# Performance work log

Hardware: AMD Instinct MI355X
Metric: run time of the kernel (lower is better)

Reference implementation:

```python
import jax, jax.numpy as jnp
import numpy as np

D = 64          # d_in
NH = [256, 256] # nn_depth_design
L = 16          # flow_layers
B = 32768       # batch of samples


def _build_masks():
    # Deterministic mask maps: this_min=0, this_max=d_in-1 for all layers
    mh0 = np.arange(NH[0]) % (D - 1)
    mh1 = np.arange(NH[1]) % (D - 1)
    M1 = (mh0[None, :] <= mh1[:, None]).astype(np.float32)  # [nh1, nh0]
    M0s, M2s = [], []
    for l in range(L):
        perm = np.arange(D) if l % 2 == 0 else np.arange(D)[::-1]
        M0s.append((perm[None, :] <= mh0[:, None]).astype(np.float32))  # [nh0, D]
        M2s.append((mh1[None, :] < perm[:, None]).astype(np.float32))  # [D, nh1]
    M0 = np.stack(M0s)                                   # [L, nh0, D]
    M1 = np.broadcast_to(M1, (L,) + M1.shape).copy()     # [L, nh1, nh0]
    M2 = np.stack(M2s)                                   # [L, D, nh1]
    return jnp.asarray(M0), jnp.asarray(M1), jnp.asarray(M2)


def setup_inputs() -> dict:
    key = jax.random.key(0)
    ks = jax.random.split(key, 13)
    u = jax.random.normal(ks[0], (B, D), dtype=jnp.float32)

    def w(k, shape, fan_in):
        return jax.random.uniform(k, shape, jnp.float32, -1.0, 1.0) / np.sqrt(fan_in)

    inp = {"u": u}
    i = 1
    for net in ("loc", "scale"):
        inp[f"{net}_W0"] = w(ks[i], (L, NH[0], D), D); i += 1
        inp[f"{net}_b0"] = w(ks[i], (L, NH[0]), D); i += 1
        inp[f"{net}_W1"] = w(ks[i], (L, NH[1], NH[0]), NH[0]); i += 1
        inp[f"{net}_b1"] = w(ks[i], (L, NH[1]), NH[0]); i += 1
        inp[f"{net}_W2"] = w(ks[i], (L, D, NH[1]), NH[1]); i += 1
        inp[f"{net}_b2"] = w(ks[i], (L, D), NH[1]); i += 1
    M0, M1, M2 = _build_masks()
    inp["M0"], inp["M1"], inp["M2"] = M0, M1, M2
    return inp


def reference(u, loc_W0, loc_b0, loc_W1, loc_b1, loc_W2, loc_b2,
              scale_W0, scale_b0, scale_W1, scale_b1, scale_W2, scale_b2,
              M0, M1, M2):
    def step(y, p):
        (lW0, lb0, lW1, lb1, lW2, lb2,
         sW0, sb0, sW1, sb1, sW2, sb2, m0, m1, m2) = p

        def net(W0, b0, W1, b1, W2, b2):
            h = jax.nn.relu(y @ (m0 * W0).T + b0)    # [B, nh0]
            h = jax.nn.relu(h @ (m1 * W1).T + b1)    # [B, nh1]
            return h @ (m2 * W2).T + b2              # [B, D]

        loc = net(lW0, lb0, lW1, lb1, lW2, lb2)
        sc = net(sW0, sb0, sW1, sb1, sW2, sb2)
        # inverse=False coupling: exp(-scale) * (y - loc)
        return jnp.exp(-sc) * (y - loc), None

    params = (loc_W0, loc_b0, loc_W1, loc_b1, loc_W2, loc_b2,
              scale_W0, scale_b0, scale_W1, scale_b1, scale_W2, scale_b2,
              M0, M1, M2)
    y, _ = jax.lax.scan(step, u, params)
    return y
```

## Files before the change

### kernel.cpp

```cpp
#include <hip/hip_runtime.h>
#include <hip/hip_bf16.h>

typedef __bf16 bf16x8 __attribute__((ext_vector_type(8)));
typedef __bf16 bf16x4 __attribute__((ext_vector_type(4)));
typedef float  f32x4  __attribute__((ext_vector_type(4)));

#define LAYERS 16
#define DIM 64
#define NHID 256
#define BATCH 32768
#define MTILE 64
#define NBLOCKS (BATCH / MTILE)

#define W0P_PER 16384
#define W1P_PER 65536
#define W2P_PER 16384
#define W0P_TOT (32 * W0P_PER)
#define W1P_TOT (32 * W1P_PER)
#define W2P_TOT (32 * W2P_PER)
#define PACK_TOT (W0P_TOT + W1P_TOT + W2P_TOT)

__device__ __forceinline__ bf16x8 ldw(const __bf16* p) { return *(const bf16x8*)p; }

__device__ __forceinline__ void lds_barrier() {
    asm volatile("s_waitcnt lgkmcnt(0)" ::: "memory");
    __builtin_amdgcn_s_barrier();
    asm volatile("" ::: "memory");
}

__global__ __launch_bounds__(256) void pack_weights(
    const float* __restrict__ lW0, const float* __restrict__ lW1, const float* __restrict__ lW2,
    const float* __restrict__ sW0, const float* __restrict__ sW1, const float* __restrict__ sW2,
    __bf16* __restrict__ ws)
{
    const long i = ((long)blockIdx.x * 256 + threadIdx.x) * 8;
    const float* W; long src; int l, n, k, which;
    if (i < W0P_TOT) {
        int netl = (int)(i / W0P_PER), rem = (int)(i % W0P_PER);
        int net = netl >> 4; l = netl & 15;
        int nt = rem >> 10, kt = (rem >> 9) & 1, lane = (rem >> 3) & 63;
        n = nt * 16 + (lane & 15); k = kt * 32 + (lane >> 4) * 8;
        W = net ? sW0 : lW0; which = 0;
        src = (long)(l * 256 + n) * 64 + k;
    } else if (i < W0P_TOT + W1P_TOT) {
        long r = i - W0P_TOT;
        int netl = (int)(r / W1P_PER), rem = (int)(r % W1P_PER);
        int net = netl >> 4; l = netl & 15;
        int nt = rem >> 12, kt = (rem >> 9) & 7, lane = (rem >> 3) & 63;
        n = nt * 16 + (lane & 15); k = kt * 32 + (lane >> 4) * 8;
        W = net ? sW1 : lW1; which = 1;
        src = (long)(l * 256 + n) * 256 + k;
    } else {
        long r = i - W0P_TOT - W1P_TOT;
        int netl = (int)(r / W2P_PER), rem = (int)(r % W2P_PER);
        int net = netl >> 4; l = netl & 15;
        int nt = rem >> 12, kt = (rem >> 9) & 7, lane = (rem >> 3) & 63;
        n = nt * 16 + (lane & 15); k = kt * 32 + (lane >> 4) * 8;
        W = net ? sW2 : lW2; which = 2;
        src = (long)(l * 64 + n) * 256 + k;
    }
    f32x4 wa = *(const f32x4*)(W + src);
    f32x4 wb = *(const f32x4*)(W + src + 4);
    const int nm = n % 63;
    const int pn = (l & 1) ? 63 - n : n;
    bf16x8 o;
    #pragma unroll
    for (int j = 0; j < 8; ++j) {
        int kk = k + j;
        bool m;
        if (which == 0)      { int pk = (l & 1) ? 63 - kk : kk; m = (pk <= nm); }
        else if (which == 1) { m = ((kk % 63) <= nm); }
        else                 { m = ((kk % 63) < pn); }
        float v = (j < 4) ? wa[j] : wb[j - 4];
        o[j] = m ? (__bf16)v : (__bf16)0.0f;
    }
    *(bf16x8*)(ws + i) = o;
}

__global__ void __attribute__((amdgpu_flat_work_group_size(512, 512)))
                __attribute__((amdgpu_waves_per_eu(4)))
flow_kernel(
    const float* __restrict__ u,
    const __bf16* __restrict__ wp,
    const float* __restrict__ lb0, const float* __restrict__ lb1, const float* __restrict__ lb2,
    const float* __restrict__ sb0, const float* __restrict__ sb1, const float* __restrict__ sb2,
    float* __restrict__ out)
{
    __shared__ __bf16 ybf[4 * 2 * 512];
    __shared__ __bf16 buf1[4 * 8 * 512];
    __shared__ __bf16 buf2[4 * 8 * 512];

    const int tid  = threadIdx.x;
    const int w    = tid >> 6;
    const int lane = tid & 63;
    const int quad = lane >> 4;
    const int l16  = lane & 15;
    const int blk  = blockIdx.x;

    const int qh = quad >> 1;
    const int qp = (quad & 1) * 4;

    const int otD = w >> 1;
    const int bh  = w & 1;

    const __bf16* w0p = wp;
    const __bf16* w1p = wp + W0P_TOT;
    const __bf16* w2p = wp + W0P_TOT + W1P_TOT;

    f32x4 y[2];
    #pragma unroll
    for (int bt = 0; bt < 2; ++bt)
        y[bt] = *(const f32x4*)(u + (long)(blk * MTILE + bh * 32 + bt * 16 + l16) * DIM
                                  + otD * 16 + quad * 4);

    const int ktY = w >> 2;
    const int flY = ((((w >> 1) & 1) * 2 + qh) * 16 + l16);

    bf16x8 wg1[4];
    #pragma unroll
    for (int oi = 0; oi < 2; ++oi)
        #pragma unroll
        for (int kt = 0; kt < 2; ++kt)
            wg1[oi * 2 + kt] = ldw(w0p + (long)((2 * w + oi) * 2 + kt) * 512 + lane * 8);

    for (int l = 0; l < LAYERS; ++l) {
        #pragma unroll
        for (int bt = 0; bt < 2; ++bt) {
            bf16x4 v;
            #pragma unroll
            for (int r = 0; r < 4; ++r) v[r] = (__bf16)y[bt][r];
            *(bf16x4*)&ybf[(((bh * 2 + bt) * 2 + ktY) * 64 + flY) * 8 + qp] = v;
        }
        lds_barrier();

        #pragma unroll
        for (int net = 0; net < 2; ++net) {
            const __bf16* w1b = w1p + (long)(net * 16 + l) * W1P_PER;
            const __bf16* w2b = w2p + (long)(net * 16 + l) * W2P_PER;
            const __bf16* w0n = w0p + (long)(net == 0 ? 16 + l : l + 1) * W0P_PER;
            const float* b0 = (net ? sb0 : lb0) + l * 256;
            const float* b1 = (net ? sb1 : lb1) + l * 256;
            const float* b2 = (net ? sb2 : lb2) + l * 64;

            bf16x8 wg2a[8];

            {
                f32x4 acc[2][4];
                #pragma unroll
                for (int oi = 0; oi < 2; ++oi)
                    #pragma unroll
                    for (int bt = 0; bt < 4; ++bt)
                        acc[oi][bt] = (f32x4){0.f, 0.f, 0.f, 0.f};
                #pragma unroll
                for (int kt = 0; kt < 2; ++kt) {
                    bf16x8 bv[4];
                    #pragma unroll
                    for (int bt = 0; bt < 4; ++bt)
                        bv[bt] = *(const bf16x8*)&ybf[((bt * 2 + kt) * 64 + lane) * 8];
                    #pragma unroll
                    for (int oi = 0; oi < 2; ++oi)
                        #pragma unroll
                        for (int bt = 0; bt < 4; ++bt)
                            acc[oi][bt] = __builtin_amdgcn_mfma_f32_16x16x32_bf16(wg1[oi * 2 + kt], bv[bt], acc[oi][bt], 0, 0, 0);
                }
                #pragma unroll
                for (int kt = 0; kt < 4; ++kt)
                    #pragma unroll
                    for (int oi = 0; oi < 2; ++oi)
                        wg2a[kt * 2 + oi] = ldw(w1b + (long)((2 * w + oi) * 8 + kt) * 512 + lane * 8);
                #pragma unroll
                for (int oi = 0; oi < 2; ++oi) {
                    f32x4 bias = *(const f32x4*)(b0 + (2 * w + oi) * 16 + quad * 4);
                    const int fl = ((oi * 2 + qh) * 16 + l16);
                    #pragma unroll
                    for (int bt = 0; bt < 4; ++bt) {
                        bf16x4 v;
                        #pragma unroll
                        for (int r = 0; r < 4; ++r)
                            v[r] = (__bf16)fmaxf(acc[oi][bt][r] + bias[r], 0.f);
                        *(bf16x4*)&buf1[((bt * 8 + w) * 64 + fl) * 8 + qp] = v;
                    }
                }
            }
            lds_barrier();

            bf16x8 wg3[8];

            {
                f32x4 acc[2][4];
                #pragma unroll
                for (int oi = 0; oi < 2; ++oi)
                    #pragma unroll
                    for (int bt = 0; bt < 4; ++bt)
                        acc[oi][bt] = (f32x4){0.f, 0.f, 0.f, 0.f};
                #pragma unroll
                for (int kt = 0; kt < 8; ++kt) {
                    bf16x8 aw[2];
                    #pragma unroll
                    for (int oi = 0; oi < 2; ++oi)
                        aw[oi] = (kt < 4) ? wg2a[kt * 2 + oi]
                                          : ldw(w1b + (long)((2 * w + oi) * 8 + kt) * 512 + lane * 8);
                    bf16x8 bv[4];
                    #pragma unroll
                    for (int bt = 0; bt < 4; ++bt)
                        bv[bt] = *(const bf16x8*)&buf1[((bt * 8 + kt) * 64 + lane) * 8];
                    #pragma unroll
                    for (int oi = 0; oi < 2; ++oi)
                        #pragma unroll
                        for (int bt = 0; bt < 4; ++bt)
                            acc[oi][bt] = __builtin_amdgcn_mfma_f32_16x16x32_bf16(aw[oi], bv[bt], acc[oi][bt], 0, 0, 0);
                }
                #pragma unroll
                for (int oi = 0; oi < 2; ++oi) {
                    f32x4 bias = *(const f32x4*)(b1 + (2 * w + oi) * 16 + quad * 4);
                    const int fl = ((oi * 2 + qh) * 16 + l16);
                    #pragma unroll
                    for (int bt = 0; bt < 4; ++bt) {
                        bf16x4 v;
                        #pragma unroll
                        for (int r = 0; r < 4; ++r)
                            v[r] = (__bf16)fmaxf(acc[oi][bt][r] + bias[r], 0.f);
                        *(bf16x4*)&buf2[((bt * 8 + w) * 64 + fl) * 8 + qp] = v;
                    }
                }
                #pragma unroll
                for (int kt = 0; kt < 8; ++kt)
                    wg3[kt] = ldw(w2b + (long)(otD * 8 + kt) * 512 + lane * 8);
            }
            lds_barrier();

            {
                f32x4 acc3[2];
                #pragma unroll
                for (int bt = 0; bt < 2; ++bt)
                    acc3[bt] = (f32x4){0.f, 0.f, 0.f, 0.f};
                #pragma unroll
                for (int kt = 0; kt < 8; ++kt) {
                    #pragma unroll
                    for (int bt = 0; bt < 2; ++bt) {
                        bf16x8 bv = *(const bf16x8*)&buf2[(((bh * 2 + bt) * 8 + kt) * 64 + lane) * 8];
                        acc3[bt] = __builtin_amdgcn_mfma_f32_16x16x32_bf16(wg3[kt], bv, acc3[bt], 0, 0, 0);
                    }
                }
                #pragma unroll
                for (int oi = 0; oi < 2; ++oi)
                    #pragma unroll
                    for (int kt = 0; kt < 2; ++kt)
                        wg1[oi * 2 + kt] = ldw(w0n + (long)((2 * w + oi) * 2 + kt) * 512 + lane * 8);
                f32x4 bias = *(const f32x4*)(b2 + otD * 16 + quad * 4);
                if (net == 0) {
                    #pragma unroll
                    for (int bt = 0; bt < 2; ++bt)
                        #pragma unroll
                        for (int r = 0; r < 4; ++r)
                            y[bt][r] -= (acc3[bt][r] + bias[r]);
                } else {
                    #pragma unroll
                    for (int bt = 0; bt < 2; ++bt)
                        #pragma unroll
                        for (int r = 0; r < 4; ++r)
                            y[bt][r] = __expf(-(acc3[bt][r] + bias[r])) * y[bt][r];
                }
            }
        }
    }

    #pragma unroll
    for (int bt = 0; bt < 2; ++bt)
        *(f32x4*)(out + (long)(blk * MTILE + bh * 32 + bt * 16 + l16) * DIM
                      + otD * 16 + quad * 4) = y[bt];
}

extern "C" void kernel_launch(void* const* d_in, const int* in_sizes, int n_in,
                              void* d_out, int out_size, void* d_ws, size_t ws_size,
                              hipStream_t stream) {
    const float* u   = (const float*)d_in[0];
    const float* lW0 = (const float*)d_in[1];
    const float* lb0 = (const float*)d_in[2];
    const float* lW1 = (const float*)d_in[3];
    const float* lb1 = (const float*)d_in[4];
    const float* lW2 = (const float*)d_in[5];
    const float* lb2 = (const float*)d_in[6];
    const float* sW0 = (const float*)d_in[7];
    const float* sb0 = (const float*)d_in[8];
    const float* sW1 = (const float*)d_in[9];
    const float* sb1 = (const float*)d_in[10];
    const float* sW2 = (const float*)d_in[11];
    const float* sb2 = (const float*)d_in[12];

    if (ws_size < (size_t)PACK_TOT * sizeof(__bf16)) return;
    __bf16* ws = (__bf16*)d_ws;

    pack_weights<<<PACK_TOT / 8 / 256, 256, 0, stream>>>(
        lW0, lW1, lW2, sW0, sW1, sW2, ws);
    flow_kernel<<<NBLOCKS, 512, 0, stream>>>(
        u, ws, lb0, lb1, lb2, sb0, sb1, sb2, (float*)d_out);
}
```

Before: 299.4 us.

## Process loc and scale nets together per layer with half-size batch tiles

The batch tile drops from 64 to 32 rows and the loc and scale MLPs now run concurrently within one pass per layer, with waves split across the two nets instead of looping over them. Weights are repacked so each layer's loc and scale matrices sit together, and the second and third layer weight loads are software-pipelined through a rotating register buffer. This halves the number of barriers per layer and doubles the block count, at the cost of more weight traffic per sample because each block now covers fewer rows.

```diff
diff --git a/kernel.cpp b/kernel.cpp
--- a/kernel.cpp
+++ b/kernel.cpp
@@ -9,15 +9,15 @@
 #define DIM 64
 #define NHID 256
 #define BATCH 32768
-#define MTILE 64
+#define MTILE 32
 #define NBLOCKS (BATCH / MTILE)
 
-#define W0P_PER 16384
-#define W1P_PER 65536
-#define W2P_PER 16384
-#define W0P_TOT (32 * W0P_PER)
-#define W1P_TOT (32 * W1P_PER)
-#define W2P_TOT (32 * W2P_PER)
+#define W0P_PER 32768
+#define W1P_PER 131072
+#define W2P_PER 32768
+#define W0P_TOT (16 * W0P_PER)
+#define W1P_TOT (16 * W1P_PER)
+#define W2P_TOT (16 * W2P_PER)
 #define PACK_TOT (W0P_TOT + W1P_TOT + W2P_TOT)
 
 __device__ __forceinline__ bf16x8 ldw(const __bf16* p) { return *(const bf16x8*)p; }
@@ -36,26 +36,26 @@
     const long i = ((long)blockIdx.x * 256 + threadIdx.x) * 8;
     const float* W; long src; int l, n, k, which;
     if (i < W0P_TOT) {
-        int netl = (int)(i / W0P_PER), rem = (int)(i % W0P_PER);
-        int net = netl >> 4; l = netl & 15;
-        int nt = rem >> 10, kt = (rem >> 9) & 1, lane = (rem >> 3) & 63;
-        n = nt * 16 + (lane & 15); k = kt * 32 + (lane >> 4) * 8;
+        l = (int)(i / W0P_PER); int rem = (int)(i % W0P_PER);
+        int g = rem >> 3, lane = g & 63, kt = (g >> 6) & 1, ot = g >> 7;
+        int net = ot >> 4;
+        n = (ot & 15) * 16 + (lane & 15); k = kt * 32 + (lane >> 4) * 8;
         W = net ? sW0 : lW0; which = 0;
         src = (long)(l * 256 + n) * 64 + k;
     } else if (i < W0P_TOT + W1P_TOT) {
         long r = i - W0P_TOT;
-        int netl = (int)(r / W1P_PER), rem = (int)(r % W1P_PER);
-        int net = netl >> 4; l = netl & 15;
-        int nt = rem >> 12, kt = (rem >> 9) & 7, lane = (rem >> 3) & 63;
-        n = nt * 16 + (lane & 15); k = kt * 32 + (lane >> 4) * 8;
+        l = (int)(r / W1P_PER); int rem = (int)(r % W1P_PER);
+        int g = rem >> 3, lane = g & 63, kt = (g >> 6) & 7, ot = g >> 9;
+        int net = ot >> 4;
+        n = (ot & 15) * 16 + (lane & 15); k = kt * 32 + (lane >> 4) * 8;
         W = net ? sW1 : lW1; which = 1;
         src = (long)(l * 256 + n) * 256 + k;
     } else {
         long r = i - W0P_TOT - W1P_TOT;
-        int netl = (int)(r / W2P_PER), rem = (int)(r % W2P_PER);
-        int net = netl >> 4; l = netl & 15;
-        int nt = rem >> 12, kt = (rem >> 9) & 7, lane = (rem >> 3) & 63;
-        n = nt * 16 + (lane & 15); k = kt * 32 + (lane >> 4) * 8;
+        l = (int)(r / W2P_PER); int rem = (int)(r % W2P_PER);
+        int g = rem >> 3, lane = g & 63, kt = (g >> 6) & 7, ot = g >> 9;
+        int net = ot >> 2;
+        n = (ot & 3) * 16 + (lane & 15); k = kt * 32 + (lane >> 4) * 8;
         W = net ? sW2 : lW2; which = 2;
         src = (long)(l * 64 + n) * 256 + k;
     }
@@ -86,9 +86,9 @@
     const float* __restrict__ sb0, const float* __restrict__ sb1, const float* __restrict__ sb2,
     float* __restrict__ out)
 {
-    __shared__ __bf16 ybf[4 * 2 * 512];
-    __shared__ __bf16 buf1[4 * 8 * 512];
-    __shared__ __bf16 buf2[4 * 8 * 512];
+    __shared__ __bf16 ybf[2 * 2 * 512];
+    __shared__ __bf16 buf1[2 * 16 * 512];
+    __shared__ __bf16 buf2[2 * 16 * 512];
 
     const int tid  = threadIdx.x;
     const int w    = tid >> 6;
@@ -100,175 +100,159 @@
     const int qh = quad >> 1;
     const int qp = (quad & 1) * 4;
 
-    const int otD = w >> 1;
-    const int bh  = w & 1;
+    const int d    = w >> 1;
+    const int h    = w & 1;
+    const int net2 = w >> 2;
+    const int wm   = w & 3;
 
     const __bf16* w0p = wp;
     const __bf16* w1p = wp + W0P_TOT;
     const __bf16* w2p = wp + W0P_TOT + W1P_TOT;
 
-    f32x4 y[2];
+    f32x4 y = *(const f32x4*)(u + (long)(blk * MTILE + h * 16 + l16) * DIM
+                                + d * 16 + quad * 4);
+
+    const int ktY = d >> 1;
+    const int flY = ((d & 1) * 2 + qh) * 16 + l16;
+
+    bf16x8 wg1[8];
     #pragma unroll
-    for (int bt = 0; bt < 2; ++bt)
-        y[bt] = *(const f32x4*)(u + (long)(blk * MTILE + bh * 32 + bt * 16 + l16) * DIM
-                                  + otD * 16 + quad * 4);
-
-    const int ktY = w >> 2;
-    const int flY = ((((w >> 1) & 1) * 2 + qh) * 16 + l16);
-
-    bf16x8 wg1[4];
-    #pragma unroll
-    for (int oi = 0; oi < 2; ++oi)
+    for (int oi = 0; oi < 4; ++oi)
         #pragma unroll
         for (int kt = 0; kt < 2; ++kt)
-            wg1[oi * 2 + kt] = ldw(w0p + (long)((2 * w + oi) * 2 + kt) * 512 + lane * 8);
+            wg1[oi * 2 + kt] = ldw(w0p + (long)((4 * w + oi) * 2 + kt) * 512 + lane * 8);
 
     for (int l = 0; l < LAYERS; ++l) {
-        #pragma unroll
-        for (int bt = 0; bt < 2; ++bt) {
+        {
             bf16x4 v;
             #pragma unroll
-            for (int r = 0; r < 4; ++r) v[r] = (__bf16)y[bt][r];
-            *(bf16x4*)&ybf[(((bh * 2 + bt) * 2 + ktY) * 64 + flY) * 8 + qp] = v;
+            for (int r = 0; r < 4; ++r) v[r] = (__bf16)y[r];
+            *(bf16x4*)&ybf[((h * 2 + ktY) * 64 + flY) * 8 + qp] = v;
         }
         lds_barrier();
 
-        #pragma unroll
-        for (int net = 0; net < 2; ++net) {
-            const __bf16* w1b = w1p + (long)(net * 16 + l) * W1P_PER;
-            const __bf16* w2b = w2p + (long)(net * 16 + l) * W2P_PER;
-            const __bf16* w0n = w0p + (long)(net == 0 ? 16 + l : l + 1) * W0P_PER;
-            const float* b0 = (net ? sb0 : lb0) + l * 256;
-            const float* b1 = (net ? sb1 : lb1) + l * 256;
-            const float* b2 = (net ? sb2 : lb2) + l * 64;
-
-            bf16x8 wg2a[8];
-
-            {
-                f32x4 acc[2][4];
-                #pragma unroll
-                for (int oi = 0; oi < 2; ++oi)
-                    #pragma unroll
-                    for (int bt = 0; bt < 4; ++bt)
-                        acc[oi][bt] = (f32x4){0.f, 0.f, 0.f, 0.f};
-                #pragma unroll
-                for (int kt = 0; kt < 2; ++kt) {
-                    bf16x8 bv[4];
-                    #pragma unroll
-                    for (int bt = 0; bt < 4; ++bt)
-                        bv[bt] = *(const bf16x8*)&ybf[((bt * 2 + kt) * 64 + lane) * 8];
-                    #pragma unroll
-                    for (int oi = 0; oi < 2; ++oi)
-                        #pragma unroll
-                        for (int bt = 0; bt < 4; ++bt)
-                            acc[oi][bt] = __builtin_amdgcn_mfma_f32_16x16x32_bf16(wg1[oi * 2 + kt], bv[bt], acc[oi][bt], 0, 0, 0);
-                }
-                #pragma unroll
-                for (int kt = 0; kt < 4; ++kt)
-                    #pragma unroll
-                    for (int oi = 0; oi < 2; ++oi)
-                        wg2a[kt * 2 + oi] = ldw(w1b + (long)((2 * w + oi) * 8 + kt) * 512 + lane * 8);
-                #pragma unroll
-                for (int oi = 0; oi < 2; ++oi) {
-                    f32x4 bias = *(const f32x4*)(b0 + (2 * w + oi) * 16 + quad * 4);
-                    const int fl = ((oi * 2 + qh) * 16 + l16);
-                    #pragma unroll
-                    for (int bt = 0; bt < 4; ++bt) {
-                        bf16x4 v;
-                        #pragma unroll
-                        for (int r = 0; r < 4; ++r)
-                            v[r] = (__bf16)fmaxf(acc[oi][bt][r] + bias[r], 0.f);
-                        *(bf16x4*)&buf1[((bt * 8 + w) * 64 + fl) * 8 + qp] = v;
-                    }
-                }
-            }
-            lds_barrier();
-
-            bf16x8 wg3[8];
-
-            {
-                f32x4 acc[2][4];
-                #pragma unroll
-                for (int oi = 0; oi < 2; ++oi)
-                    #pragma unroll
-                    for (int bt = 0; bt < 4; ++bt)
-                        acc[oi][bt] = (f32x4){0.f, 0.f, 0.f, 0.f};
-                #pragma unroll
-                for (int kt = 0; kt < 8; ++kt) {
-                    bf16x8 aw[2];
-                    #pragma unroll
-                    for (int oi = 0; oi < 2; ++oi)
-                        aw[oi] = (kt < 4) ? wg2a[kt * 2 + oi]
-                                          : ldw(w1b + (long)((2 * w + oi) * 8 + kt) * 512 + lane * 8);
-                    bf16x8 bv[4];
-                    #pragma unroll
-                    for (int bt = 0; bt < 4; ++bt)
-                        bv[bt] = *(const bf16x8*)&buf1[((bt * 8 + kt) * 64 + lane) * 8];
-                    #pragma unroll
-                    for (int oi = 0; oi < 2; ++oi)
-                        #pragma unroll
-                        for (int bt = 0; bt < 4; ++bt)
-                            acc[oi][bt] = __builtin_amdgcn_mfma_f32_16x16x32_bf16(aw[oi], bv[bt], acc[oi][bt], 0, 0, 0);
-                }
-                #pragma unroll
-                for (int oi = 0; oi < 2; ++oi) {
-                    f32x4 bias = *(const f32x4*)(b1 + (2 * w + oi) * 16 + quad * 4);
-                    const int fl = ((oi * 2 + qh) * 16 + l16);
-                    #pragma unroll
-                    for (int bt = 0; bt < 4; ++bt) {
-                        bf16x4 v;
-                        #pragma unroll
-                        for (int r = 0; r < 4; ++r)
-                            v[r] = (__bf16)fmaxf(acc[oi][bt][r] + bias[r], 0.f);
-                        *(bf16x4*)&buf2[((bt * 8 + w) * 64 + fl) * 8 + qp] = v;
-                    }
-                }
-                #pragma unroll
-                for (int kt = 0; kt < 8; ++kt)
-                    wg3[kt] = ldw(w2b + (long)(otD * 8 + kt) * 512 + lane * 8);
-            }
-            lds_barrier();
-
-            {
-                f32x4 acc3[2];
+        const __bf16* w1b = w1p + (long)l * W1P_PER;
+        const __bf16* w2b = w2p + (long)l * W2P_PER;
+        const __bf16* w0n = w0p + (long)(l + 1) * W0P_PER;
+        const float* b0 = (net2 ? sb0 : lb0) + l * 256;
+        const float* b1 = (net2 ? sb1 : lb1) + l * 256;
+
+        bf16x8 wg2a[12];
+
+        {
+            f32x4 acc[4][2];
+            #pragma unroll
+            for (int oi = 0; oi < 4; ++oi)
                 #pragma unroll
                 for (int bt = 0; bt < 2; ++bt)
-                    acc3[bt] = (f32x4){0.f, 0.f, 0.f, 0.f};
-                #pragma unroll
-                for (int kt = 0; kt < 8; ++kt) {
-                    #pragma unroll
-                    for (int bt = 0; bt < 2; ++bt) {
-                        bf16x8 bv = *(const bf16x8*)&buf2[(((bh * 2 + bt) * 8 + kt) * 64 + lane) * 8];
-                        acc3[bt] = __builtin_amdgcn_mfma_f32_16x16x32_bf16(wg3[kt], bv, acc3[bt], 0, 0, 0);
-                    }
-                }
-                #pragma unroll
-                for (int oi = 0; oi < 2; ++oi)
-                    #pragma unroll
-                    for (int kt = 0; kt < 2; ++kt)
-                        wg1[oi * 2 + kt] = ldw(w0n + (long)((2 * w + oi) * 2 + kt) * 512 + lane * 8);
-                f32x4 bias = *(const f32x4*)(b2 + otD * 16 + quad * 4);
-                if (net == 0) {
-                    #pragma unroll
-                    for (int bt = 0; bt < 2; ++bt)
-                        #pragma unroll
-                        for (int r = 0; r < 4; ++r)
-                            y[bt][r] -= (acc3[bt][r] + bias[r]);
-                } else {
-                    #pragma unroll
-                    for (int bt = 0; bt < 2; ++bt)
-                        #pragma unroll
-                        for (int r = 0; r < 4; ++r)
-                            y[bt][r] = __expf(-(acc3[bt][r] + bias[r])) * y[bt][r];
-                }
-            }
+                    acc[oi][bt] = (f32x4){0.f, 0.f, 0.f, 0.f};
+            #pragma unroll
+            for (int kt = 0; kt < 2; ++kt)
+                #pragma unroll
+                for (int bt = 0; bt < 2; ++bt) {
+                    bf16x8 bv = *(const bf16x8*)&ybf[((bt * 2 + kt) * 64 + lane) * 8];
+                    #pragma unroll
+                    for (int oi = 0; oi < 4; ++oi)
+                        acc[oi][bt] = __builtin_amdgcn_mfma_f32_16x16x32_bf16(wg1[oi * 2 + kt], bv, acc[oi][bt], 0, 0, 0);
+                }
+            #pragma unroll
+            for (int s = 0; s < 3; ++s)
+                #pragma unroll
+                for (int oi = 0; oi < 4; ++oi)
+                    wg2a[s * 4 + oi] = ldw(w1b + (long)((4 * w + oi) * 8 + s) * 512 + lane * 8);
+            #pragma unroll
+            for (int oi = 0; oi < 4; ++oi) {
+                const int kt1 = 2 * wm + (oi >> 1) + 8 * net2;
+                const int fl  = ((oi & 1) * 2 + qh) * 16 + l16;
+                f32x4 bias = *(const f32x4*)(b0 + (4 * wm + oi) * 16 + quad * 4);
+                #pragma unroll
+                for (int bt = 0; bt < 2; ++bt) {
+                    bf16x4 v;
+                    #pragma unroll
+                    for (int r = 0; r < 4; ++r)
+                        v[r] = (__bf16)fmaxf(acc[oi][bt][r] + bias[r], 0.f);
+                    *(bf16x4*)&buf1[((bt * 16 + kt1) * 64 + fl) * 8 + qp] = v;
+                }
+            }
+        }
+        lds_barrier();
+
+        bf16x8 wg3[8];
+
+        {
+            f32x4 acc[4][2];
+            #pragma unroll
+            for (int oi = 0; oi < 4; ++oi)
+                #pragma unroll
+                for (int bt = 0; bt < 2; ++bt)
+                    acc[oi][bt] = (f32x4){0.f, 0.f, 0.f, 0.f};
+            #pragma unroll
+            for (int kt = 0; kt < 8; ++kt) {
+                const int slot = kt % 3;
+                #pragma unroll
+                for (int bt = 0; bt < 2; ++bt) {
+                    bf16x8 bv = *(const bf16x8*)&buf1[((bt * 16 + net2 * 8 + kt) * 64 + lane) * 8];
+                    #pragma unroll
+                    for (int oi = 0; oi < 4; ++oi)
+                        acc[oi][bt] = __builtin_amdgcn_mfma_f32_16x16x32_bf16(wg2a[slot * 4 + oi], bv, acc[oi][bt], 0, 0, 0);
+                }
+                if (kt < 5) {
+                    #pragma unroll
+                    for (int oi = 0; oi < 4; ++oi)
+                        wg2a[slot * 4 + oi] = ldw(w1b + (long)((4 * w + oi) * 8 + (kt + 3)) * 512 + lane * 8);
+                }
+            }
+            #pragma unroll
+            for (int oi = 0; oi < 4; ++oi) {
+                const int kt1 = 2 * wm + (oi >> 1) + 8 * net2;
+                const int fl  = ((oi & 1) * 2 + qh) * 16 + l16;
+                f32x4 bias = *(const f32x4*)(b1 + (4 * wm + oi) * 16 + quad * 4);
+                #pragma unroll
+                for (int bt = 0; bt < 2; ++bt) {
+                    bf16x4 v;
+                    #pragma unroll
+                    for (int r = 0; r < 4; ++r)
+                        v[r] = (__bf16)fmaxf(acc[oi][bt][r] + bias[r], 0.f);
+                    *(bf16x4*)&buf2[((bt * 16 + kt1) * 64 + fl) * 8 + qp] = v;
+                }
+            }
+            #pragma unroll
+            for (int o2 = 0; o2 < 2; ++o2)
+                #pragma unroll
+                for (int s = 0; s < 4; ++s)
+                    wg3[o2 * 4 + s] = ldw(w2b + (long)((o2 * 4 + d) * 8 + s) * 512 + lane * 8);
+        }
+        lds_barrier();
+
+        {
+            f32x4 aL = (f32x4){0.f, 0.f, 0.f, 0.f};
+            f32x4 aS = (f32x4){0.f, 0.f, 0.f, 0.f};
+            #pragma unroll
+            for (int kt = 0; kt < 8; ++kt) {
+                bf16x8 bvL = *(const bf16x8*)&buf2[((h * 16 + kt) * 64 + lane) * 8];
+                aL = __builtin_amdgcn_mfma_f32_16x16x32_bf16(wg3[kt & 3], bvL, aL, 0, 0, 0);
+                bf16x8 bvS = *(const bf16x8*)&buf2[((h * 16 + 8 + kt) * 64 + lane) * 8];
+                aS = __builtin_amdgcn_mfma_f32_16x16x32_bf16(wg3[4 + (kt & 3)], bvS, aS, 0, 0, 0);
+                if (kt < 4) {
+                    wg3[kt]     = ldw(w2b + (long)(d * 8 + (kt + 4)) * 512 + lane * 8);
+                    wg3[4 + kt] = ldw(w2b + (long)((4 + d) * 8 + (kt + 4)) * 512 + lane * 8);
+                }
+            }
+            #pragma unroll
+            for (int oi = 0; oi < 4; ++oi)
+                #pragma unroll
+                for (int kt = 0; kt < 2; ++kt)
+                    wg1[oi * 2 + kt] = ldw(w0n + (long)((4 * w + oi) * 2 + kt) * 512 + lane * 8);
+            f32x4 bL = *(const f32x4*)(lb2 + l * 64 + d * 16 + quad * 4);
+            f32x4 bS = *(const f32x4*)(sb2 + l * 64 + d * 16 + quad * 4);
+            #pragma unroll
+            for (int r = 0; r < 4; ++r)
+                y[r] = __expf(-(aS[r] + bS[r])) * (y[r] - (aL[r] + bL[r]));
         }
     }
 
-    #pragma unroll
-    for (int bt = 0; bt < 2; ++bt)
-        *(f32x4*)(out + (long)(blk * MTILE + bh * 32 + bt * 16 + l16) * DIM
-                      + otD * 16 + quad * 4) = y[bt];
+    *(f32x4*)(out + (long)(blk * MTILE + h * 16 + l16) * DIM
+                  + d * 16 + quad * 4) = y;
 }
 
 extern "C" void kernel_launch(void* const* d_in, const int* in_sizes, int n_in,
```

New measurement: 388.9 us. 29.9% more time.
